# Kernel tuning notes

Measured on AMD Instinct MI355X. Metric: run time of the kernel, lower is better.

## Reference

```python
import jax, jax.numpy as jnp
import numpy as np

KH = KW = 3
SH = SW = 1
PH = PW = 1


def _im2col(x, kh, kw, sh, sw, ph, pw):
    # x: [N, C, H, W] -> cols: [N, C*kh*kw, H_out*W_out], ordering (C, kh, kw)
    N, C, H, W = x.shape
    H_out = (H + 2 * ph - kh) // sh + 1
    W_out = (W + 2 * pw - kw) // sw + 1
    x_pad = jnp.pad(x, ((0, 0), (0, 0), (ph, ph), (pw, pw)))
    # fixed small loop over kernel offsets (kh*kw = 9), strided slices
    patches = [x_pad[:, :, i:i + sh * H_out:sh, j:j + sw * W_out:sw]
               for i in range(kh) for j in range(kw)]  # each [N, C, H_out, W_out]
    cols = jnp.stack(patches, axis=2)  # [N, C, kh*kw, H_out, W_out]
    cols = cols.reshape(N, C * kh * kw, H_out * W_out)
    return cols, H_out, W_out


def setup_inputs() -> dict:
    key = jax.random.key(0)
    k1, k2, k3 = jax.random.split(key, 3)
    x = jax.random.normal(k1, (16, 128, 56, 56), dtype=jnp.float32)
    weight = jax.random.normal(k2, (256, 128, 3, 3), dtype=jnp.float32) * 0.05
    fan_in = 128 * 3 * 3
    bound = 1.0 / fan_in ** 0.5
    bias = jax.random.uniform(k3, (256,), dtype=jnp.float32, minval=-bound, maxval=bound)
    return {"x": x, "weight": weight, "bias": bias}


def reference(x, weight, bias):
    # im2col unfold + (analog) matmul conv; noise_cfg=None -> plain matmul
    cols, H_out, W_out = _im2col(x, KH, KW, SH, SW, PH, PW)  # [N, K, L]
    N = cols.shape[0]
    Cout = weight.shape[0]
    Wmat = weight.reshape(Cout, -1)  # [Cout, K], K = C*kh*kw
    # y[n, l, o] = sum_k cols[n, k, l] * Wmat[o, k]  (AnalogMatMulFn without noise)
    y = jnp.einsum('nkl,ok->nol', cols, Wmat)  # [N, Cout, L]
    y = y.reshape(N, Cout, H_out, W_out)
    y = y + bias[None, :, None, None]
    return y
```

## Files before the change

kernel.cpp:

```cpp
#include <hip/hip_runtime.h>
#include <hip/hip_bf16.h>
#include <stdint.h>


typedef __attribute__((ext_vector_type(8))) short short8;
typedef __attribute__((ext_vector_type(4))) float floatx4;

__device__ static inline void gload_lds16(const void* g, void* l) {
  typedef const __attribute__((address_space(1))) unsigned int* gp_t;
  typedef __attribute__((address_space(3))) unsigned int* lp_t;
  __builtin_amdgcn_global_load_lds((gp_t)(uintptr_t)g, (lp_t)(uint32_t)(uintptr_t)l,
                                   16, 0, 0);
}

__global__ __launch_bounds__(256)
void pre_kernel(const float* __restrict__ x, const float* __restrict__ wsrc,
                __hip_bfloat16* __restrict__ xp, __hip_bfloat16* __restrict__ wt) {
  const int b = blockIdx.x;
  if (b < 16 * 58) {
    const int n = b / 58, hp = b % 58;
    __hip_bfloat16* dst = xp + (size_t)(n * 58 + hp) * 58 * 128;
    if (hp == 0 || hp == 57) {
      const uint4 z = {0, 0, 0, 0};
      uint4* p = (uint4*)dst;
      for (int i = threadIdx.x; i < 928; i += 256) p[i] = z;
      return;
    }
    const int h = hp - 1;
    __shared__ float tile[128][57];
    const float* src = x + (size_t)n * (128 * 3136) + h * 56;
    for (int i = threadIdx.x; i < 128 * 14; i += 256) {
      const int c = i / 14, q = i - c * 14;
      const float4 v = ((const float4*)(src + (size_t)c * 3136))[q];
      tile[c][4 * q + 0] = v.x;
      tile[c][4 * q + 1] = v.y;
      tile[c][4 * q + 2] = v.z;
      tile[c][4 * q + 3] = v.w;
    }
    __syncthreads();
    if (threadIdx.x < 32) {
      const uint4 z = {0, 0, 0, 0};
      const int col = (threadIdx.x >> 4) * 57;
      ((uint4*)(dst + (size_t)col * 128))[threadIdx.x & 15] = z;
    }
    __hip_bfloat16* di = dst + 128;
    for (int i = threadIdx.x; i < 56 * 16; i += 256) {
      const int w = i >> 4, c8 = (i & 15) * 8;
      union { uint4 u; __hip_bfloat16 hh[8]; } pk;
#pragma unroll
      for (int j = 0; j < 8; ++j) pk.hh[j] = __float2bfloat16(tile[c8 + j][w]);
      *(uint4*)(di + (size_t)w * 128 + c8) = pk.u;
    }
  } else {
    const int base = (b - 928) * 256 + threadIdx.x;
    for (int t = base; t < 256 * 9 * 128; t += 36 * 256) {
      const int c = t & 127;
      const int kq = (t >> 7) % 9;
      const int cout = t / (9 * 128);
      wt[t] = __float2bfloat16(wsrc[(size_t)(cout * 128 + c) * 9 + kq]);
    }
  }
}

__global__ __launch_bounds__(256)
void conv_gemm_kernel(const __hip_bfloat16* __restrict__ xp,
                      const __hip_bfloat16* __restrict__ wt,
                      const float* __restrict__ bias,
                      float* __restrict__ out) {
  __shared__ __align__(16) char smem[49152 + 2 * 16384];

  const int tid = threadIdx.x;
  const int lane = tid & 63;
  const int wave = tid >> 6;
  const int wm = wave >> 1, wn = wave & 1;

  const int id = blockIdx.x;
  const int xcd = id & 7;
  const int r = id >> 3;
  const int mt_ = r / 98;
  const int nt_ = xcd * 98 + (r - mt_ * 98);
  const int m0 = mt_ * 128;
  const int n0 = nt_ * 64;

  const int nimg0 = n0 / 3136;
  const int rem0 = n0 - nimg0 * 3136;
  const int hh0 = rem0 / 56;
  const int ww0 = rem0 - hh0 * 56;
  const int P0 = (nimg0 * 58 + hh0) * 58 + ww0;
  const char* pbase = (const char*)xp + (size_t)P0 * 256;

  const char* wtb = (const char*)wt;
  const char* gA[4];
#pragma unroll
  for (int i = 0; i < 4; ++i) {
    const int f = (i * 256 + tid) * 16;
    const int rowA = f >> 7;
    const int sub = (f >> 4) & 7;
    gA[i] = wtb + (size_t)(m0 + rowA) * 2304 + ((sub ^ (rowA & 7)) << 4);
  }
#pragma unroll
  for (int i = 0; i < 12; ++i) {
    const int j = i * 256 + tid;
    const int row = j >> 4;
    const int slot = j & 15;
    gload_lds16(pbase + row * 256 + ((slot ^ (row & 7)) << 4),
                smem + i * 4096 + wave * 1024);
  }
#pragma unroll
  for (int i = 0; i < 4; ++i)
    gload_lds16(gA[i], smem + 49152 + i * 4096 + wave * 1024);

  const int col = lane & 15;
  const int quad = lane >> 4;
  const int x7 = lane & 7;
  const int arow = (wm * 64 + col) * 128;
  int cko[2];
  cko[0] = ((0 + quad) ^ x7) << 4;
  cko[1] = ((4 + quad) ^ x7) << 4;
  int rbase[2];
#pragma unroll
  for (int nt = 0; nt < 2; ++nt) {
    const int pix = n0 + wn * 32 + nt * 16 + col;
    const int ni = pix / 3136;
    const int re = pix - ni * 3136;
    const int ph = re / 56;
    const int pw = re - ph * 56;
    rbase[nt] = (ni * 58 + ph) * 58 + pw - P0;
  }

  floatx4 acc[4][2];
#pragma unroll
  for (int a = 0; a < 4; ++a)
#pragma unroll
    for (int c = 0; c < 2; ++c) acc[a][c] = (floatx4)0.f;

#pragma unroll 1
  for (int s = 0; s < 18; ++s) {
    __syncthreads();
    if (s < 17) {
      const int s1 = s + 1;
      const int aofs = (s1 >> 1) * 256 + (s1 & 1) * 128;
      char* ad = smem + 49152 + ((s1 & 1) << 14) + wave * 1024;
#pragma unroll
      for (int i = 0; i < 4; ++i)
        gload_lds16(gA[i] + aofs, ad + i * 4096);
    }
    const int kq = s >> 1, ch = s & 1;
    const int kh = kq / 3;
    const int tofs = kh * 58 + (kq - kh * 3);
    const char* ab = smem + 49152 + ((s & 1) << 14);
#pragma unroll
    for (int ks = 0; ks < 2; ++ks) {
      short8 af[4], bf[2];
#pragma unroll
      for (int mt = 0; mt < 4; ++mt)
        af[mt] = *(const short8*)(ab + arow + mt * 2048 + cko[ks]);
      const int cB = ch * 8 + ks * 4 + quad;
#pragma unroll
      for (int nt = 0; nt < 2; ++nt) {
        const int rowB = rbase[nt] + tofs;
        const int pos = cB ^ (rowB & 7);
        bf[nt] = *(const short8*)(smem + rowB * 256 + (pos << 4));
      }
#pragma unroll
      for (int mt = 0; mt < 4; ++mt)
#pragma unroll
        for (int nt = 0; nt < 2; ++nt)
          acc[mt][nt] = __builtin_amdgcn_mfma_f32_16x16x32_bf16(
              af[mt], bf[nt], acc[mt][nt], 0, 0, 0);
    }
  }

  const int rb = quad * 4;
#pragma unroll
  for (int nt = 0; nt < 2; ++nt) {
    const int pix = n0 + wn * 32 + nt * 16 + col;
    const int nimg = pix / 3136;
    const int rem = pix - nimg * 3136;
    float* op = out + (size_t)nimg * (256 * 3136) + rem;
#pragma unroll
    for (int mt = 0; mt < 4; ++mt) {
      const int mb = m0 + wm * 64 + mt * 16 + rb;
#pragma unroll
      for (int rr = 0; rr < 4; ++rr) {
        op[(size_t)(mb + rr) * 3136] = acc[mt][nt][rr] + bias[mb + rr];
      }
    }
  }
}

__global__ __launch_bounds__(256)
void direct_conv_kernel(const float* __restrict__ x, const float* __restrict__ wgt,
                        const float* __restrict__ bias, float* __restrict__ out) {
  const long t = (long)blockIdx.x * 256 + threadIdx.x;
  if (t >= 16L * 256 * 3136) return;
  const int w = t % 56;
  const int h = (t / 56) % 56;
  const int o = (t / 3136) % 256;
  const int n = t / (256L * 3136);
  float s = bias[o];
  for (int c = 0; c < 128; ++c)
    for (int kh = 0; kh < 3; ++kh) {
      const int hh = h + kh - 1;
      if (hh < 0 || hh >= 56) continue;
      for (int kw = 0; kw < 3; ++kw) {
        const int ww = w + kw - 1;
        if (ww < 0 || ww >= 56) continue;
        s += x[((size_t)(n * 128 + c) * 56 + hh) * 56 + ww] *
             wgt[((size_t)(o * 128 + c) * 3 + kh) * 3 + kw];
      }
    }
  out[t] = s;
}

extern "C" void kernel_launch(void* const* d_in, const int* in_sizes, int n_in,
                              void* d_out, int out_size, void* d_ws, size_t ws_size,
                              hipStream_t stream) {
  const float* x = (const float*)d_in[0];
  const float* w = (const float*)d_in[1];
  const float* b = (const float*)d_in[2];
  float* out = (float*)d_out;

  const size_t xp_bytes = (size_t)16 * 58 * 58 * 128 * 2;
  const size_t wt_bytes = (size_t)256 * 9 * 128 * 2;

  if (ws_size >= xp_bytes + wt_bytes) {
    __hip_bfloat16* xp = (__hip_bfloat16*)d_ws;
    __hip_bfloat16* wt = (__hip_bfloat16*)((char*)d_ws + xp_bytes);
    hipLaunchKernelGGL(pre_kernel, dim3(16 * 58 + 36), dim3(256), 0, stream,
                       x, w, xp, wt);
    hipLaunchKernelGGL(conv_gemm_kernel, dim3(1568), dim3(256), 0, stream,
                       xp, wt, b, out);
  } else {
    const long total = 16L * 256 * 3136;
    hipLaunchKernelGGL(direct_conv_kernel, dim3((unsigned)((total + 255) / 256)),
                       dim3(256), 0, stream, x, w, b, out);
  }
}
```

Measured before the change: 132.2 us.

## Load weight fragments directly into registers using MFMA-ready packed layout

The weight prepack now writes weights in an order that matches the MFMA 16x16x32 fragment layout, so each wave can load its A fragments straight from global memory into registers with double buffering. This removes the LDS staging for weights and the per-step barrier. LDS use drops to 48KB, and launch bounds request 3 blocks per SM. Wave tiling changes from 2x2 (64x32) to 4x1 (32x64 per wave), so every wave now reads all 64 pixel columns of B from LDS. The trade-off is more global/L2 traffic per wave and more LDS reads of B.

```diff
diff --git a/kernel.cpp b/kernel.cpp
--- a/kernel.cpp
+++ b/kernel.cpp
@@ -54,25 +54,33 @@
   } else {
     const int base = (b - 928) * 256 + threadIdx.x;
     for (int t = base; t < 256 * 9 * 128; t += 36 * 256) {
-      const int c = t & 127;
-      const int kq = (t >> 7) % 9;
-      const int cout = t / (9 * 128);
+      const int e = t & 7;
+      const int rr = (t >> 3) & 15;
+      const int q = (t >> 7) & 3;
+      const int ks = (t >> 9) & 1;
+      const int ch = (t >> 10) & 1;
+      const int t11 = t >> 11;
+      const int kq = t11 % 9;
+      const int g = t11 / 9;
+      const int cout = g * 16 + rr;
+      const int c = ch * 64 + ks * 32 + q * 8 + e;
       wt[t] = __float2bfloat16(wsrc[(size_t)(cout * 128 + c) * 9 + kq]);
     }
   }
 }
 
-__global__ __launch_bounds__(256)
+__global__ __launch_bounds__(256, 3)
 void conv_gemm_kernel(const __hip_bfloat16* __restrict__ xp,
                       const __hip_bfloat16* __restrict__ wt,
                       const float* __restrict__ bias,
                       float* __restrict__ out) {
-  __shared__ __align__(16) char smem[49152 + 2 * 16384];
+  __shared__ __align__(16) char smem[49152];
 
   const int tid = threadIdx.x;
   const int lane = tid & 63;
   const int wave = tid >> 6;
-  const int wm = wave >> 1, wn = wave & 1;
+  const int col = lane & 15;
+  const int quad = lane >> 4;
 
   const int id = blockIdx.x;
   const int xcd = id & 7;
@@ -89,15 +97,6 @@
   const int P0 = (nimg0 * 58 + hh0) * 58 + ww0;
   const char* pbase = (const char*)xp + (size_t)P0 * 256;
 
-  const char* wtb = (const char*)wt;
-  const char* gA[4];
-#pragma unroll
-  for (int i = 0; i < 4; ++i) {
-    const int f = (i * 256 + tid) * 16;
-    const int rowA = f >> 7;
-    const int sub = (f >> 4) & 7;
-    gA[i] = wtb + (size_t)(m0 + rowA) * 2304 + ((sub ^ (rowA & 7)) << 4);
-  }
 #pragma unroll
   for (int i = 0; i < 12; ++i) {
     const int j = i * 256 + tid;
@@ -106,21 +105,23 @@
     gload_lds16(pbase + row * 256 + ((slot ^ (row & 7)) << 4),
                 smem + i * 4096 + wave * 1024);
   }
-#pragma unroll
-  for (int i = 0; i < 4; ++i)
-    gload_lds16(gA[i], smem + 49152 + i * 4096 + wave * 1024);
-
-  const int col = lane & 15;
-  const int quad = lane >> 4;
-  const int x7 = lane & 7;
-  const int arow = (wm * 64 + col) * 128;
-  int cko[2];
-  cko[0] = ((0 + quad) ^ x7) << 4;
-  cko[1] = ((4 + quad) ^ x7) << 4;
-  int rbase[2];
-#pragma unroll
-  for (int nt = 0; nt < 2; ++nt) {
-    const int pix = n0 + wn * 32 + nt * 16 + col;
+
+  const char* wtb = (const char*)wt;
+  const int gbase = (m0 >> 4) + wave * 2;
+  const char* pA0 = wtb + (size_t)gbase * 36864 + lane * 16;
+  const char* pA1 = pA0 + 36864;
+
+  short8 areg[2][2][2];
+#pragma unroll
+  for (int ks = 0; ks < 2; ++ks) {
+    areg[0][0][ks] = *(const short8*)(pA0 + ks * 1024);
+    areg[0][1][ks] = *(const short8*)(pA1 + ks * 1024);
+  }
+
+  int rbase[4];
+#pragma unroll
+  for (int nt = 0; nt < 4; ++nt) {
+    const int pix = n0 + nt * 16 + col;
     const int ni = pix / 3136;
     const int re = pix - ni * 3136;
     const int ph = re / 56;
@@ -128,59 +129,60 @@
     rbase[nt] = (ni * 58 + ph) * 58 + pw - P0;
   }
 
-  floatx4 acc[4][2];
-#pragma unroll
-  for (int a = 0; a < 4; ++a)
-#pragma unroll
-    for (int c = 0; c < 2; ++c) acc[a][c] = (floatx4)0.f;
-
-#pragma unroll 1
+  floatx4 acc[2][4];
+#pragma unroll
+  for (int a = 0; a < 2; ++a)
+#pragma unroll
+    for (int c = 0; c < 4; ++c) acc[a][c] = (floatx4)0.f;
+
+  __syncthreads();
+
+#pragma unroll
   for (int s = 0; s < 18; ++s) {
-    __syncthreads();
+    const int cur = s & 1, nxt = cur ^ 1;
     if (s < 17) {
       const int s1 = s + 1;
-      const int aofs = (s1 >> 1) * 256 + (s1 & 1) * 128;
-      char* ad = smem + 49152 + ((s1 & 1) << 14) + wave * 1024;
-#pragma unroll
-      for (int i = 0; i < 4; ++i)
-        gload_lds16(gA[i] + aofs, ad + i * 4096);
+      const int ofs = (s1 >> 1) * 4096 + (s1 & 1) * 2048;
+#pragma unroll
+      for (int ks = 0; ks < 2; ++ks) {
+        areg[nxt][0][ks] = *(const short8*)(pA0 + ofs + ks * 1024);
+        areg[nxt][1][ks] = *(const short8*)(pA1 + ofs + ks * 1024);
+      }
     }
     const int kq = s >> 1, ch = s & 1;
     const int kh = kq / 3;
     const int tofs = kh * 58 + (kq - kh * 3);
-    const char* ab = smem + 49152 + ((s & 1) << 14);
-#pragma unroll
-    for (int ks = 0; ks < 2; ++ks) {
-      short8 af[4], bf[2];
-#pragma unroll
-      for (int mt = 0; mt < 4; ++mt)
-        af[mt] = *(const short8*)(ab + arow + mt * 2048 + cko[ks]);
-      const int cB = ch * 8 + ks * 4 + quad;
-#pragma unroll
-      for (int nt = 0; nt < 2; ++nt) {
-        const int rowB = rbase[nt] + tofs;
+    short8 bf[4][2];
+#pragma unroll
+    for (int nt = 0; nt < 4; ++nt) {
+      const int rowB = rbase[nt] + tofs;
+#pragma unroll
+      for (int ks = 0; ks < 2; ++ks) {
+        const int cB = ch * 8 + ks * 4 + quad;
         const int pos = cB ^ (rowB & 7);
-        bf[nt] = *(const short8*)(smem + rowB * 256 + (pos << 4));
-      }
-#pragma unroll
-      for (int mt = 0; mt < 4; ++mt)
-#pragma unroll
-        for (int nt = 0; nt < 2; ++nt)
+        bf[nt][ks] = *(const short8*)(smem + rowB * 256 + (pos << 4));
+      }
+    }
+#pragma unroll
+    for (int ks = 0; ks < 2; ++ks)
+#pragma unroll
+      for (int mt = 0; mt < 2; ++mt)
+#pragma unroll
+        for (int nt = 0; nt < 4; ++nt)
           acc[mt][nt] = __builtin_amdgcn_mfma_f32_16x16x32_bf16(
-              af[mt], bf[nt], acc[mt][nt], 0, 0, 0);
-    }
+              areg[cur][mt][ks], bf[nt][ks], acc[mt][nt], 0, 0, 0);
   }
 
   const int rb = quad * 4;
 #pragma unroll
-  for (int nt = 0; nt < 2; ++nt) {
-    const int pix = n0 + wn * 32 + nt * 16 + col;
+  for (int nt = 0; nt < 4; ++nt) {
+    const int pix = n0 + nt * 16 + col;
     const int nimg = pix / 3136;
     const int rem = pix - nimg * 3136;
     float* op = out + (size_t)nimg * (256 * 3136) + rem;
 #pragma unroll
-    for (int mt = 0; mt < 4; ++mt) {
-      const int mb = m0 + wm * 64 + mt * 16 + rb;
+    for (int mt = 0; mt < 2; ++mt) {
+      const int mb = m0 + wave * 32 + mt * 16 + rb;
 #pragma unroll
       for (int rr = 0; rr < 4; ++rr) {
         op[(size_t)(mb + rr) * 3136] = acc[mt][nt][rr] + bias[mb + rr];
```

Result: faster. 125.8 us (-4.8%).
